# Kernel optimization log

Hardware: AMD Instinct MI355X
Metric: run time of the kernel (lower is better)

## Reference

```python
import jax, jax.numpy as jnp
import numpy as np

B = 64        # number of queries (eg_idx groups)
E_PER = 4096  # edges per group (uniform, sorted by eg_idx)
D = 256       # embedding dim (n_dims_in)
K = 50        # max_edges (top-k per group)
E = B * E_PER


def setup_inputs() -> dict:
    key = jax.random.key(0)
    ks = jax.random.split(key, 10)
    eg = jnp.repeat(jnp.arange(B, dtype=jnp.int32), E_PER)  # sorted group ids
    mid = jax.random.randint(ks[0], (E, 7), 0, 1000, dtype=jnp.int32)
    # (eg_idx, vi, ti, vj, tj, rel, node_i, node_j, query_idx); col0 sorted, col8 = query id
    selected_edges = jnp.concatenate([eg[:, None], mid, eg[:, None]], axis=1)
    return {
        "step_score_add_all": jnp.ones((3, 1), jnp.float32),
        "visited_nodes_reg": jax.random.normal(ks[1], (E,), jnp.float32),
        "src_ts_emb_special_set": jax.random.normal(ks[2], (3, D), jnp.float32),
        "sample_loss": jax.random.normal(ks[3], (E,), jnp.float32),
        "node_rep_vi": jax.random.normal(ks[4], (E, D), jnp.float32),
        "node_rep_vj": jax.random.normal(ks[5], (E, D), jnp.float32),
        "rel_emb": jax.random.normal(ks[6], (E, D), jnp.float32),
        "query_src_ts_emb": jax.random.normal(ks[7], (B, D), jnp.float32),
        "query_rel_emb": jax.random.normal(ks[8], (B, D), jnp.float32),
        "selected_edges": selected_edges,
        "max_edges": K,
    }


def reference(step_score_add_all, visited_nodes_reg, src_ts_emb_special_set,
              sample_loss, node_rep_vi, node_rep_vj, rel_emb,
              query_src_ts_emb, query_rel_emb, selected_edges, max_edges):
    qidx = selected_edges[:, 8]                      # (E,) per-edge query index
    q_src = query_src_ts_emb[qidx]                   # (E, D) gather
    q_rel = query_rel_emb[qidx]                      # (E, D) gather
    # G3.forward: L1 norms along feature dim (src_ts_emb_special_set unused by G3 math)
    triple_loss = jnp.sum(jnp.abs(q_src + rel_emb - node_rep_vj), axis=1)  # (E,)
    rel_loss = jnp.sum(jnp.abs(q_rel - rel_emb), axis=1)                   # (E,)
    # stack (rel_loss, sample_loss, triple_loss) and contract with -|w| (3,1)
    stacked = jnp.stack((rel_loss, sample_loss, triple_loss), axis=-1)     # (E, 3)
    target_score = (stacked @ (-jnp.abs(step_score_add_all)))[:, 0]        # (E,)
    # segmented per-eg_idx top-k; groups are uniform (E_PER) and contiguous
    scores_b = target_score.reshape(B, E_PER)
    _, idx = jax.lax.top_k(scores_b, max_edges)                            # (B, K)
    orig_indices = (jnp.arange(B, dtype=jnp.int32)[:, None] * E_PER + idx).reshape(-1)
    pruned_edges = selected_edges[orig_indices]                            # (B*K, 9)
    return target_score, visited_nodes_reg, pruned_edges, orig_indices
```

## Files before the change

### kernel.cpp

```cpp
#include <hip/hip_runtime.h>
#include <math.h>

#define BB 64
#define E_PER 4096
#define DD 256
#define KK 50
#define EE (BB * E_PER)

__global__ __launch_bounds__(256) void score_kernel(
    const float* __restrict__ w3,
    const float* __restrict__ sample_loss,
    const float* __restrict__ vj,
    const float* __restrict__ rel,
    const float* __restrict__ qsrc,
    const float* __restrict__ qrel,
    const int*   __restrict__ edges,
    float* __restrict__ score_out)
{
    const int gwave = (blockIdx.x * blockDim.x + threadIdx.x) >> 6;
    const int lane  = threadIdx.x & 63;
    if (gwave >= EE) return;
    const int e = gwave;
    const int b = edges[(size_t)e * 9 + 8];

    const float4 r  = ((const float4*)(rel  + (size_t)e * DD))[lane];
    const float4 v  = ((const float4*)(vj   + (size_t)e * DD))[lane];
    const float4 qs = ((const float4*)(qsrc + (size_t)b * DD))[lane];
    const float4 qr = ((const float4*)(qrel + (size_t)b * DD))[lane];

    const float w0 = fabsf(w3[0]);
    const float w1 = fabsf(w3[1]);
    const float w2 = fabsf(w3[2]);

    float relp = fabsf(qr.x - r.x) + fabsf(qr.y - r.y) +
                 fabsf(qr.z - r.z) + fabsf(qr.w - r.w);
    float trip = fabsf(qs.x + r.x - v.x) + fabsf(qs.y + r.y - v.y) +
                 fabsf(qs.z + r.z - v.z) + fabsf(qs.w + r.w - v.w);

    float p = w0 * relp + w2 * trip;
    #pragma unroll
    for (int m = 1; m < 64; m <<= 1) p += __shfl_xor(p, m, 64);

    if (lane == 0) score_out[e] = -(p + w1 * sample_loss[e]);
}

__global__ __launch_bounds__(256) void copy_kernel(
    const float* __restrict__ in, float* __restrict__ out)
{
    const int i = blockIdx.x * blockDim.x + threadIdx.x;
    if (i < EE / 4) ((float4*)out)[i] = ((const float4*)in)[i];
}

__global__ __launch_bounds__(256) void topk_kernel(
    const float* __restrict__ scores,
    const int*   __restrict__ edges,
    float* __restrict__ pruned_out,
    float* __restrict__ orig_out)
{
    __shared__ float s_val[E_PER];
    __shared__ float s_red_v[4];
    __shared__ int   s_red_i[4];
    __shared__ int   s_sel[KK];

    const int b   = blockIdx.x;
    const int tid = threadIdx.x;

    const float4* src = (const float4*)(scores + (size_t)b * E_PER);
    for (int i = tid; i < E_PER / 4; i += 256)
        ((float4*)s_val)[i] = src[i];
    __syncthreads();

    const int lane = tid & 63;
    const int wid  = tid >> 6;

    for (int k = 0; k < KK; ++k) {
        float bv = -INFINITY;
        int   bi = 0x7fffffff;
        for (int i = tid; i < E_PER; i += 256) {
            float v = s_val[i];
            if (v > bv) { bv = v; bi = i; }
        }
        #pragma unroll
        for (int m = 1; m < 64; m <<= 1) {
            float ov = __shfl_xor(bv, m, 64);
            int   oi = __shfl_xor(bi, m, 64);
            if (ov > bv || (ov == bv && oi < bi)) { bv = ov; bi = oi; }
        }
        if (lane == 0) { s_red_v[wid] = bv; s_red_i[wid] = bi; }
        __syncthreads();
        if (tid == 0) {
            float fv = s_red_v[0]; int fi = s_red_i[0];
            #pragma unroll
            for (int w = 1; w < 4; ++w) {
                if (s_red_v[w] > fv || (s_red_v[w] == fv && s_red_i[w] < fi)) {
                    fv = s_red_v[w]; fi = s_red_i[w];
                }
            }
            s_sel[k] = fi;
            s_val[fi] = -INFINITY;
        }
        __syncthreads();
    }

    for (int t = tid; t < KK * 9; t += 256) {
        const int k = t / 9, j = t % 9;
        const int orig = b * E_PER + s_sel[k];
        pruned_out[(size_t)(b * KK + k) * 9 + j] = (float)edges[(size_t)orig * 9 + j];
    }
    for (int t = tid; t < KK; t += 256)
        orig_out[b * KK + t] = (float)(b * E_PER + s_sel[t]);
}

extern "C" void kernel_launch(void* const* d_in, const int* in_sizes, int n_in,
                              void* d_out, int out_size, void* d_ws, size_t ws_size,
                              hipStream_t stream) {
    const float* w        = (const float*)d_in[0];
    const float* visited  = (const float*)d_in[1];
    const float* sample   = (const float*)d_in[3];
    const float* vj       = (const float*)d_in[5];
    const float* rel      = (const float*)d_in[6];
    const float* qsrc     = (const float*)d_in[7];
    const float* qrel     = (const float*)d_in[8];
    const int*   edges    = (const int*)d_in[9];

    float* out        = (float*)d_out;
    float* score_out  = out;
    float* visited_out= out + EE;
    float* pruned_out = out + 2 * EE;
    float* orig_out   = out + 2 * EE + BB * KK * 9;

    score_kernel<<<EE / 4, 256, 0, stream>>>(w, sample, vj, rel, qsrc, qrel,
                                             edges, score_out);
    copy_kernel<<<(EE / 4 + 255) / 256, 256, 0, stream>>>(visited, visited_out);
    topk_kernel<<<BB, 256, 0, stream>>>(score_out, edges, pruned_out, orig_out);
}
```

Measured before the change: 694.3 us.

## Use register-resident per-wave top-k with a merge pass, and fuse the copy into the score kernel

The top-k kernel used to run 50 rounds of block-wide argmax over shared memory, each with two __syncthreads. Now each wave keeps its 1024 scores in registers, finds its own top-50 with no block barriers, and a single wave then merges the 200 candidates. The separate copy of visited_nodes_reg is folded into the first 256 blocks of the score kernel, which saves one launch. Tie-breaking still prefers the lower index, but the code now depends on exact index matching to clear the selected element.

```diff
diff --git a/kernel.cpp b/kernel.cpp
--- a/kernel.cpp
+++ b/kernel.cpp
@@ -7,7 +7,9 @@
 #define KK 50
 #define EE (BB * E_PER)
 
-__global__ __launch_bounds__(256) void score_kernel(
+typedef float f4 __attribute__((ext_vector_type(4)));
+
+__global__ __launch_bounds__(256) void score_copy_kernel(
     const float* __restrict__ w3,
     const float* __restrict__ sample_loss,
     const float* __restrict__ vj,
@@ -15,18 +17,25 @@
     const float* __restrict__ qsrc,
     const float* __restrict__ qrel,
     const int*   __restrict__ edges,
+    const float* __restrict__ visited,
+    float* __restrict__ visited_out,
     float* __restrict__ score_out)
 {
+    if (blockIdx.x < 256) {
+        const int t = blockIdx.x * 256 + threadIdx.x;
+        ((f4*)visited_out)[t] = ((const f4*)visited)[t];
+    }
+
     const int gwave = (blockIdx.x * blockDim.x + threadIdx.x) >> 6;
     const int lane  = threadIdx.x & 63;
     if (gwave >= EE) return;
     const int e = gwave;
     const int b = edges[(size_t)e * 9 + 8];
 
-    const float4 r  = ((const float4*)(rel  + (size_t)e * DD))[lane];
-    const float4 v  = ((const float4*)(vj   + (size_t)e * DD))[lane];
-    const float4 qs = ((const float4*)(qsrc + (size_t)b * DD))[lane];
-    const float4 qr = ((const float4*)(qrel + (size_t)b * DD))[lane];
+    const f4 r  = ((const f4*)(rel  + (size_t)e * DD))[lane];
+    const f4 v  = ((const f4*)(vj   + (size_t)e * DD))[lane];
+    const f4 qs = ((const f4*)(qsrc + (size_t)b * DD))[lane];
+    const f4 qr = ((const f4*)(qrel + (size_t)b * DD))[lane];
 
     const float w0 = fabsf(w3[0]);
     const float w1 = fabsf(w3[1]);
@@ -44,63 +53,87 @@
     if (lane == 0) score_out[e] = -(p + w1 * sample_loss[e]);
 }
 
-__global__ __launch_bounds__(256) void copy_kernel(
-    const float* __restrict__ in, float* __restrict__ out)
-{
-    const int i = blockIdx.x * blockDim.x + threadIdx.x;
-    if (i < EE / 4) ((float4*)out)[i] = ((const float4*)in)[i];
-}
-
 __global__ __launch_bounds__(256) void topk_kernel(
     const float* __restrict__ scores,
     const int*   __restrict__ edges,
     float* __restrict__ pruned_out,
     float* __restrict__ orig_out)
 {
-    __shared__ float s_val[E_PER];
-    __shared__ float s_red_v[4];
-    __shared__ int   s_red_i[4];
+    __shared__ float cand_v[4 * KK];
+    __shared__ int   cand_i[4 * KK];
     __shared__ int   s_sel[KK];
 
-    const int b   = blockIdx.x;
-    const int tid = threadIdx.x;
-
-    const float4* src = (const float4*)(scores + (size_t)b * E_PER);
-    for (int i = tid; i < E_PER / 4; i += 256)
-        ((float4*)s_val)[i] = src[i];
-    __syncthreads();
-
+    const int b    = blockIdx.x;
+    const int tid  = threadIdx.x;
     const int lane = tid & 63;
     const int wid  = tid >> 6;
+
+    const int cb = wid * 1024;
+    const f4* src = (const f4*)(scores + (size_t)b * E_PER) + (cb >> 2) + lane;
+    f4 c0 = src[0];
+    f4 c1 = src[64];
+    f4 c2 = src[128];
+    f4 c3 = src[192];
+    const int ibase = cb + 4 * lane;
 
     for (int k = 0; k < KK; ++k) {
         float bv = -INFINITY;
         int   bi = 0x7fffffff;
-        for (int i = tid; i < E_PER; i += 256) {
-            float v = s_val[i];
-            if (v > bv) { bv = v; bi = i; }
-        }
+        #define SCAN(vec, q) \
+            if (vec.x > bv) { bv = vec.x; bi = ibase + 256*q + 0; } \
+            if (vec.y > bv) { bv = vec.y; bi = ibase + 256*q + 1; } \
+            if (vec.z > bv) { bv = vec.z; bi = ibase + 256*q + 2; } \
+            if (vec.w > bv) { bv = vec.w; bi = ibase + 256*q + 3; }
+        SCAN(c0, 0) SCAN(c1, 1) SCAN(c2, 2) SCAN(c3, 3)
+        #undef SCAN
+
         #pragma unroll
         for (int m = 1; m < 64; m <<= 1) {
             float ov = __shfl_xor(bv, m, 64);
             int   oi = __shfl_xor(bi, m, 64);
             if (ov > bv || (ov == bv && oi < bi)) { bv = ov; bi = oi; }
         }
-        if (lane == 0) { s_red_v[wid] = bv; s_red_i[wid] = bi; }
-        __syncthreads();
-        if (tid == 0) {
-            float fv = s_red_v[0]; int fi = s_red_i[0];
+
+        const int rel_i = bi - ibase;
+        #define CLR(vec, q) \
+            if (rel_i == 256*q + 0) vec.x = -INFINITY; \
+            if (rel_i == 256*q + 1) vec.y = -INFINITY; \
+            if (rel_i == 256*q + 2) vec.z = -INFINITY; \
+            if (rel_i == 256*q + 3) vec.w = -INFINITY;
+        CLR(c0, 0) CLR(c1, 1) CLR(c2, 2) CLR(c3, 3)
+        #undef CLR
+
+        if (lane == 0) { cand_v[wid * KK + k] = bv; cand_i[wid * KK + k] = bi; }
+    }
+    __syncthreads();
+
+    if (wid == 0) {
+        float mv[4]; int mi[4];
+        #pragma unroll
+        for (int rr = 0; rr < 4; ++rr) {
+            const int t = lane + 64 * rr;
+            const bool ok = t < 4 * KK;
+            mv[rr] = ok ? cand_v[t] : -INFINITY;
+            mi[rr] = ok ? cand_i[t] : 0x7fffffff;
+        }
+        for (int k = 0; k < KK; ++k) {
+            float bv = -INFINITY; int bi = 0x7fffffff;
             #pragma unroll
-            for (int w = 1; w < 4; ++w) {
-                if (s_red_v[w] > fv || (s_red_v[w] == fv && s_red_i[w] < fi)) {
-                    fv = s_red_v[w]; fi = s_red_i[w];
-                }
+            for (int rr = 0; rr < 4; ++rr)
+                if (mv[rr] > bv || (mv[rr] == bv && mi[rr] < bi)) { bv = mv[rr]; bi = mi[rr]; }
+            #pragma unroll
+            for (int m = 1; m < 64; m <<= 1) {
+                float ov = __shfl_xor(bv, m, 64);
+                int   oi = __shfl_xor(bi, m, 64);
+                if (ov > bv || (ov == bv && oi < bi)) { bv = ov; bi = oi; }
             }
-            s_sel[k] = fi;
-            s_val[fi] = -INFINITY;
+            #pragma unroll
+            for (int rr = 0; rr < 4; ++rr)
+                if (mi[rr] == bi) mv[rr] = -INFINITY;
+            if (lane == 0) s_sel[k] = bi;
         }
-        __syncthreads();
     }
+    __syncthreads();
 
     for (int t = tid; t < KK * 9; t += 256) {
         const int k = t / 9, j = t % 9;
@@ -129,8 +162,8 @@
     float* pruned_out = out + 2 * EE;
     float* orig_out   = out + 2 * EE + BB * KK * 9;
 
-    score_kernel<<<EE / 4, 256, 0, stream>>>(w, sample, vj, rel, qsrc, qrel,
-                                             edges, score_out);
-    copy_kernel<<<(EE / 4 + 255) / 256, 256, 0, stream>>>(visited, visited_out);
+    score_copy_kernel<<<EE / 4, 256, 0, stream>>>(w, sample, vj, rel, qsrc, qrel,
+                                                  edges, visited, visited_out,
+                                                  score_out);
     topk_kernel<<<BB, 256, 0, stream>>>(score_out, edges, pruned_out, orig_out);
 }
```

Result: no change. 693.1 us (-0.2%).
